# Optimization experiments

Measured on AMD Instinct MI355X. Metric: run time of the kernel, lower is better.

The kernel has to match this reference:

```python
import jax, jax.numpy as jnp
import numpy as np

EPS = 1e-6
ENERGY_THRESHOLD = 0.95
LS_INIT = 1e-5


def setup_inputs() -> dict:
    key = jax.random.key(0)
    k_x, k_u, k_s, k_v = jax.random.split(key, 4)
    dim, max_rank = 4096, 16
    x = jax.random.normal(k_x, (4, 2048, dim), dtype=jnp.float32)
    U = jax.random.normal(k_u, (dim, max_rank), dtype=jnp.float32) * 0.02
    S = jax.random.uniform(k_s, (max_rank,), dtype=jnp.float32)
    V = jax.random.normal(k_v, (max_rank, dim), dtype=jnp.float32) * 0.02
    norm_weight = jnp.ones((dim,), dtype=jnp.float32)
    gamma = jnp.full((dim,), LS_INIT, dtype=jnp.float32)
    return {"x": x, "U": U, "S": S, "V": V,
            "norm_weight": norm_weight, "gamma": gamma}


def _rank_mask(S):
    # Effective rank from singular-value energy (non-differentiable decision,
    # matching torch's .item() host sync which detaches it from autograd).
    s_abs = jnp.abs(S)
    cum = jnp.cumsum(s_abs) / jnp.maximum(s_abs.sum(), 1e-8)
    hit = cum >= ENERGY_THRESHOLD
    r = jnp.where(hit.any(), jnp.argmax(hit) + 1, S.shape[0])
    keep = (jnp.arange(S.shape[0]) < r).astype(S.dtype)
    return jax.lax.stop_gradient(keep)


def reference(x, U, S, V, norm_weight, gamma):
    # RMSNorm (computed in fp32, matching x.float() in torch)
    xf = x.astype(jnp.float32)
    x_norm = (xf * jax.lax.rsqrt(jnp.mean(xf * xf, axis=-1, keepdims=True) + EPS)).astype(x.dtype)
    x_norm = x_norm * norm_weight
    # Adaptive-rank low-rank projection: masking columns >= r equals slicing [:r]
    keep = _rank_mask(S)
    h = jnp.einsum('bsd,dr->bsr', x_norm, U)        # [B,S,max_rank]
    h = h * (S * keep)                               # zero out ranks >= r
    h = jnp.einsum('bsr,rd->bsd', h, V)             # [B,S,dim]
    # LayerScale + residual
    return x + h * gamma
```

## Files before the change

kernel.cpp:

```cpp
#include <hip/hip_runtime.h>

#define DIM   4096
#define RANK  16
#define BM    16
#define NT    512
#define NWAVE 8
#define KSLICE (DIM/NWAVE)
#define NKB   (KSLICE/32)
#define NCB   (DIM/16/NWAVE)

typedef __fp16 f16;
typedef __fp16 half4 __attribute__((ext_vector_type(4)));
typedef __fp16 half8 __attribute__((ext_vector_type(8)));
typedef float  floatx4 __attribute__((ext_vector_type(4)));

__global__ __launch_bounds__(256) void prep_weights(const float* __restrict__ U,
    const float* __restrict__ nw, const float* __restrict__ V,
    f16* __restrict__ Ub, f16* __restrict__ Vb)
{
    const int i   = blockIdx.x * 256 + threadIdx.x;
    const int l   = i & 63;
    const int n   = l & 15;
    const int blk = l >> 4;
    if (i < 8192) {
        const int kb = i >> 6;
        half8 u;
        #pragma unroll
        for (int e = 0; e < 8; ++e) {
            const int k = kb * 32 + blk * 8 + e;
            u[e] = (f16)(nw[k] * U[(size_t)k * RANK + n]);
        }
        *(half8*)(Ub + (size_t)i * 8) = u;
    }
    {
        const int cb = i >> 6;
        half4 v;
        #pragma unroll
        for (int e = 0; e < 4; ++e) {
            const int k = blk * 4 + e;
            v[e] = (f16)V[(size_t)k * DIM + cb * 16 + n];
        }
        *(half4*)(Vb + (size_t)i * 4) = v;
    }
}

__global__ __launch_bounds__(NT, 4) void arl_fused(
    const float* __restrict__ x,  const f16* __restrict__ Ub,
    const f16* __restrict__ Vb,   const float* __restrict__ S,
    const float* __restrict__ gamma, float* __restrict__ out)
{
    const int t   = threadIdx.x;
    const int w   = t >> 6;
    const int l   = t & 63;
    const int n   = l & 15;
    const int blk = l >> 4;
    const size_t row0 = (size_t)blockIdx.x * BM;

    __shared__ float s_hacc[NWAVE][16][17];
    __shared__ float s_ssq[NWAVE][16];
    __shared__ __align__(8) f16 s_hh[16][16];

    const float* xlane = x + (row0 + n) * DIM + w * KSLICE + blk * 8;
    const half8* UbW   = (const half8*)Ub + (size_t)w * NKB * 64 + l;

    floatx4 acc = {0.f, 0.f, 0.f, 0.f};
    float ssq = 0.f;

    float4 xa0 = *(const float4*)(xlane);
    float4 xa1 = *(const float4*)(xlane + 4);
    half8  ub  = UbW[0];

    #pragma unroll 1
    for (int kb = 0; kb < NKB; ++kb) {
        const int kn = (kb + 1) & (NKB - 1);
        float4 nx0 = *(const float4*)(xlane + kn * 32);
        float4 nx1 = *(const float4*)(xlane + kn * 32 + 4);
        half8  nub = UbW[(size_t)kn * 64];
        ssq = fmaf(xa0.x, xa0.x, ssq); ssq = fmaf(xa0.y, xa0.y, ssq);
        ssq = fmaf(xa0.z, xa0.z, ssq); ssq = fmaf(xa0.w, xa0.w, ssq);
        ssq = fmaf(xa1.x, xa1.x, ssq); ssq = fmaf(xa1.y, xa1.y, ssq);
        ssq = fmaf(xa1.z, xa1.z, ssq); ssq = fmaf(xa1.w, xa1.w, ssq);
        half8 a;
        a[0] = (f16)xa0.x; a[1] = (f16)xa0.y; a[2] = (f16)xa0.z; a[3] = (f16)xa0.w;
        a[4] = (f16)xa1.x; a[5] = (f16)xa1.y; a[6] = (f16)xa1.z; a[7] = (f16)xa1.w;
        acc = __builtin_amdgcn_mfma_f32_16x16x32_f16(a, ub, acc, 0, 0, 0);
        xa0 = nx0; xa1 = nx1; ub = nub;
    }

    ssq += __shfl_xor(ssq, 16, 64);
    ssq += __shfl_xor(ssq, 32, 64);
    if (l < 16) s_ssq[w][l] = ssq;

    #pragma unroll
    for (int j = 0; j < 4; ++j) s_hacc[w][blk * 4 + j][n] = acc[j];
    __syncthreads();

    if (t < 256) {
        const int m = t >> 4, q = t & 15;
        float hsum = 0.f, tssq = 0.f;
        #pragma unroll
        for (int ww = 0; ww < NWAVE; ++ww) {
            hsum += s_hacc[ww][m][q];
            tssq += s_ssq[ww][m];
        }
        const float rstd = rsqrtf(tssq * (1.0f / DIM) + 1e-6f);
        float tot = 0.f;
        #pragma unroll
        for (int i = 0; i < RANK; ++i) tot += fabsf(S[i]);
        const float denom = fmaxf(tot, 1e-8f);
        float cum = 0.f, se = 0.f;
        #pragma unroll
        for (int i = 0; i < RANK; ++i) {
            if (i == q) se = ((cum / denom) < 0.95f) ? S[i] : 0.f;
            cum += fabsf(S[i]);
        }
        s_hh[m][q] = (f16)(hsum * se * rstd);
    }
    __syncthreads();

    const half4 ah = *(const half4*)&s_hh[n][blk * 4];
    const half4* Vb4 = (const half4*)Vb;
    const floatx4 zero = {0.f, 0.f, 0.f, 0.f};

    #pragma unroll 2
    for (int i = 0; i < NCB; ++i) {
        const int cb = w * NCB + i;
        const int c0 = cb * 16;
        const half4 bv = Vb4[(size_t)cb * 64 + l];
        floatx4 d = __builtin_amdgcn_mfma_f32_16x16x16f16(ah, bv, zero, 0, 0, 0);
        const float g = gamma[c0 + n];
        const float* xr  = x   + (row0 + blk * 4) * DIM + c0 + n;
        float*       orr = out + (row0 + blk * 4) * DIM + c0 + n;
        #pragma unroll
        for (int j = 0; j < 4; ++j) {
            const float xv = xr[(size_t)j * DIM];
            __builtin_nontemporal_store(fmaf(g, d[j], xv), orr + (size_t)j * DIM);
        }
    }
}

extern "C" void kernel_launch(void* const* d_in, const int* in_sizes, int n_in,
                              void* d_out, int out_size, void* d_ws, size_t ws_size,
                              hipStream_t stream) {
    (void)in_sizes; (void)n_in; (void)ws_size;
    const float* x  = (const float*)d_in[0];
    const float* U  = (const float*)d_in[1];
    const float* S  = (const float*)d_in[2];
    const float* V  = (const float*)d_in[3];
    const float* nw = (const float*)d_in[4];
    const float* g  = (const float*)d_in[5];
    float* out = (float*)d_out;
    f16* Ub = (f16*)d_ws;
    f16* Vb = (f16*)((char*)d_ws + 128 * 1024);

    hipLaunchKernelGGL(prep_weights, dim3(64), dim3(256), 0, stream,
                       U, nw, V, Ub, Vb);

    const int rows = out_size / DIM;
    const int grid = rows / BM;
    hipLaunchKernelGGL(arl_fused, dim3(grid), dim3(NT), 0, stream,
                       x, Ub, Vb, S, g, out);
}
```

Baseline: 73.36 us.

## Stage x/U loads via global_load_lds double buffer and vectorize epilogue

The first GEMM loop now streams x and Ub tiles into a per-wave LDS ring with asynchronous global_load_lds and explicit vmcnt waits, replacing register prefetching, and the loop is fully unrolled. The second phase swaps the MFMA operands so each lane owns four consecutive columns of one row, which allows float4 loads of x and gamma and a single 16-byte nontemporal store in place of four strided scalar accesses. The LDS ring adds about 48KB of shared memory per block, which may lower occupancy, and the manual waitcnt sequencing risks ordering errors.

```diff
diff --git a/kernel.cpp b/kernel.cpp
--- a/kernel.cpp
+++ b/kernel.cpp
@@ -13,6 +13,15 @@
 typedef __fp16 half4 __attribute__((ext_vector_type(4)));
 typedef __fp16 half8 __attribute__((ext_vector_type(8)));
 typedef float  floatx4 __attribute__((ext_vector_type(4)));
+
+#define VM_WAIT(N) { asm volatile("s_waitcnt vmcnt(" #N ")" ::: "memory"); \
+                     __builtin_amdgcn_sched_barrier(0); }
+
+__device__ __forceinline__ void gld16(const void* g, void* l) {
+    __builtin_amdgcn_global_load_lds((__attribute__((address_space(1))) void*)g,
+                                     (__attribute__((address_space(3))) void*)l,
+                                     16, 0, 0);
+}
 
 __global__ __launch_bounds__(256) void prep_weights(const float* __restrict__ U,
     const float* __restrict__ nw, const float* __restrict__ V,
@@ -56,26 +65,40 @@
     const int blk = l >> 4;
     const size_t row0 = (size_t)blockIdx.x * BM;
 
+    __shared__ __align__(16) float ring[NWAVE][2][768];
     __shared__ float s_hacc[NWAVE][16][17];
     __shared__ float s_ssq[NWAVE][16];
     __shared__ __align__(8) f16 s_hh[16][16];
 
-    const float* xlane = x + (row0 + n) * DIM + w * KSLICE + blk * 8;
-    const half8* UbW   = (const half8*)Ub + (size_t)w * NKB * 64 + l;
+    const float* xsrc  = x + (row0 + n) * DIM + w * KSLICE + blk * 8;
+    const f16*   ubsrc = Ub + ((size_t)(w * NKB) * 64 + l) * 8;
 
     floatx4 acc = {0.f, 0.f, 0.f, 0.f};
     float ssq = 0.f;
 
-    float4 xa0 = *(const float4*)(xlane);
-    float4 xa1 = *(const float4*)(xlane + 4);
-    half8  ub  = UbW[0];
+    {
+        float* slot = &ring[w][0][0];
+        gld16(xsrc,             slot);
+        gld16(xsrc + 4,         slot + 256);
+        gld16(ubsrc,            slot + 512);
+    }
 
-    #pragma unroll 1
+    #pragma unroll
     for (int kb = 0; kb < NKB; ++kb) {
-        const int kn = (kb + 1) & (NKB - 1);
-        float4 nx0 = *(const float4*)(xlane + kn * 32);
-        float4 nx1 = *(const float4*)(xlane + kn * 32 + 4);
-        half8  nub = UbW[(size_t)kn * 64];
+        __builtin_amdgcn_sched_barrier(0);
+        if (kb + 1 < NKB) {
+            float* slot = &ring[w][(kb + 1) & 1][0];
+            gld16(xsrc + (kb + 1) * 32,      slot);
+            gld16(xsrc + (kb + 1) * 32 + 4,  slot + 256);
+            gld16(ubsrc + (size_t)(kb + 1) * 512, slot + 512);
+        }
+        if (kb < NKB - 1) VM_WAIT(3) else VM_WAIT(0)
+
+        const int s = kb & 1;
+        const float4 xa0 = *(const float4*)&ring[w][s][l * 4];
+        const float4 xa1 = *(const float4*)&ring[w][s][256 + l * 4];
+        const half8  ub  = *(const half8*)((const f16*)&ring[w][s][512] + l * 8);
+
         ssq = fmaf(xa0.x, xa0.x, ssq); ssq = fmaf(xa0.y, xa0.y, ssq);
         ssq = fmaf(xa0.z, xa0.z, ssq); ssq = fmaf(xa0.w, xa0.w, ssq);
         ssq = fmaf(xa1.x, xa1.x, ssq); ssq = fmaf(xa1.y, xa1.y, ssq);
@@ -84,7 +107,6 @@
         a[0] = (f16)xa0.x; a[1] = (f16)xa0.y; a[2] = (f16)xa0.z; a[3] = (f16)xa0.w;
         a[4] = (f16)xa1.x; a[5] = (f16)xa1.y; a[6] = (f16)xa1.z; a[7] = (f16)xa1.w;
         acc = __builtin_amdgcn_mfma_f32_16x16x32_f16(a, ub, acc, 0, 0, 0);
-        xa0 = nx0; xa1 = nx1; ub = nub;
     }
 
     ssq += __shfl_xor(ssq, 16, 64);
@@ -121,21 +143,23 @@
     const half4 ah = *(const half4*)&s_hh[n][blk * 4];
     const half4* Vb4 = (const half4*)Vb;
     const floatx4 zero = {0.f, 0.f, 0.f, 0.f};
+    const float* xrow = x   + (row0 + n) * DIM;
+    float*       orow = out + (row0 + n) * DIM;
 
-    #pragma unroll 2
+    #pragma unroll 4
     for (int i = 0; i < NCB; ++i) {
         const int cb = w * NCB + i;
-        const int c0 = cb * 16;
+        const int c0 = cb * 16 + blk * 4;
         const half4 bv = Vb4[(size_t)cb * 64 + l];
-        floatx4 d = __builtin_amdgcn_mfma_f32_16x16x16f16(ah, bv, zero, 0, 0, 0);
-        const float g = gamma[c0 + n];
-        const float* xr  = x   + (row0 + blk * 4) * DIM + c0 + n;
-        float*       orr = out + (row0 + blk * 4) * DIM + c0 + n;
-        #pragma unroll
-        for (int j = 0; j < 4; ++j) {
-            const float xv = xr[(size_t)j * DIM];
-            __builtin_nontemporal_store(fmaf(g, d[j], xv), orr + (size_t)j * DIM);
-        }
+        floatx4 d = __builtin_amdgcn_mfma_f32_16x16x16f16(bv, ah, zero, 0, 0, 0);
+        const float4 g  = *(const float4*)(gamma + c0);
+        const float4 xv = *(const float4*)(xrow + c0);
+        floatx4 o;
+        o[0] = fmaf(g.x, d[0], xv.x);
+        o[1] = fmaf(g.y, d[1], xv.y);
+        o[2] = fmaf(g.z, d[2], xv.z);
+        o[3] = fmaf(g.w, d[3], xv.w);
+        __builtin_nontemporal_store(o, (floatx4*)(orow + c0));
     }
 }
 
```

New measurement: 74.31 us. Within noise of the previous version (+1.3%).
